# Performance work log

Hardware: AMD Instinct MI355X
Metric: run time of the kernel (lower is better)

Reference implementation:

```python
import jax, jax.numpy as jnp
import numpy as np

B, N, FIN = 512, 256, 32   # batch, num_agents, (tgt_feat+rbt_feat)*2
H1, G, FOUT, K, ACT = 16, 8, 16, 3, 5  # compress dims, shared feat G, GF out, taps, actions


def setup_inputs() -> dict:
    key = jax.random.key(0)
    ks = jax.random.split(key, 10)
    x = jax.random.normal(ks[0], (B, N, FIN), dtype=jnp.float32)
    # GSO, scaled ~1/sqrt(N) so repeated shifts stay numerically tame
    S = jax.random.normal(ks[1], (B, N, N), dtype=jnp.float32) * (1.0 / np.sqrt(N))
    def lin(k, fout, fin):
        return jax.random.normal(k, (fout, fin), dtype=jnp.float32) * (1.0 / np.sqrt(fin))
    W1, b1 = lin(ks[2], H1, FIN), jnp.zeros((H1,), jnp.float32)
    W2, b2 = lin(ks[3], G, H1), jnp.zeros((G,), jnp.float32)
    # graph-filter taps: [FOUT, K, G] (E=1 folded away)
    Hgf = jax.random.normal(ks[4], (FOUT, K, G), dtype=jnp.float32) * (1.0 / np.sqrt(K * G))
    bgf = jnp.zeros((FOUT,), jnp.float32)
    Wa, ba = lin(ks[5], ACT, FOUT), jnp.zeros((ACT,), jnp.float32)
    return {"x": x, "S": S, "W1": W1, "b1": b1, "W2": W2, "b2": b2,
            "Hgf": Hgf, "bgf": bgf, "Wa": Wa, "ba": ba}


def reference(x, S, W1, b1, W2, b2, Hgf, bgf, Wa, ba):
    # compress MLP, batched over all agents at once (replaces the per-agent loop)
    h = jax.nn.relu(jnp.einsum('bnf,hf->bnh', x, W1) + b1)
    h = jax.nn.relu(jnp.einsum('bnh,gh->bng', h, W2) + b2)   # [B, N, G]
    z = jnp.transpose(h, (0, 2, 1))                          # [B, G, N]
    # K-tap graph shift: z_k = z_{k-1} @ S
    taps = [z]
    for _ in range(K - 1):
        taps.append(jnp.einsum('bgn,bnm->bgm', taps[-1], S))
    zK = jnp.stack(taps, axis=1)                             # [B, K, G, N]
    y = jnp.einsum('fkg,bkgn->bfn', Hgf, zK) + bgf[None, :, None]
    y = jax.nn.relu(y)                                       # [B, FOUT, N]
    # action MLP per agent (single linear, batched over agents)
    actions = jnp.einsum('bfn,af->bna', y, Wa) + ba          # [B, N, ACT]
    return actions
```

## Files before the change

kernel.cpp:

```cpp
#include <hip/hip_runtime.h>

constexpr int Bsz  = 512;
constexpr int Nn   = 256;
constexpr int FINc = 32;
constexpr int H1c  = 16;
constexpr int Gc   = 8;
constexpr int FOUTc= 16;
constexpr int Kc   = 3;
constexpr int ACTc = 5;

__global__ __launch_bounds__(256, 2)
void cpn_kernel(const float* __restrict__ x,  const float* __restrict__ S,
                const float* __restrict__ W1, const float* __restrict__ b1,
                const float* __restrict__ W2, const float* __restrict__ b2,
                const float* __restrict__ Hgf,const float* __restrict__ bgf,
                const float* __restrict__ Wa, const float* __restrict__ ba,
                float* __restrict__ out)
{
    const int b    = blockIdx.x;
    const int tid  = threadIdx.x;
    const int wid  = tid >> 6;
    const int lane = tid & 63;
    const int n    = tid;

    __shared__ __align__(16) float zA[Nn][Gc];
    __shared__ __align__(16) float zB[Nn][Gc];
    __shared__ __align__(16) float zpart[4][Gc][Nn];

    float xr[FINc];
    {
        const float4* xp = reinterpret_cast<const float4*>(x + ((size_t)b * Nn + n) * FINc);
        #pragma unroll
        for (int i = 0; i < FINc / 4; ++i) {
            float4 v = xp[i];
            xr[4*i+0] = v.x; xr[4*i+1] = v.y; xr[4*i+2] = v.z; xr[4*i+3] = v.w;
        }
    }
    float h1v[H1c];
    #pragma unroll
    for (int h = 0; h < H1c; ++h) {
        float a = b1[h];
        #pragma unroll
        for (int f = 0; f < FINc; ++f) a = fmaf(W1[h*FINc + f], xr[f], a);
        h1v[h] = fmaxf(a, 0.0f);
    }
    float z0r[Gc];
    #pragma unroll
    for (int g = 0; g < Gc; ++g) {
        float a = b2[g];
        #pragma unroll
        for (int h = 0; h < H1c; ++h) a = fmaf(W2[g*H1c + h], h1v[h], a);
        z0r[g] = fmaxf(a, 0.0f);
        zA[n][g] = z0r[g];
    }
    __syncthreads();

    float z1r[Gc], z2r[Gc];

    auto spass = [&](const float (*zsrc)[Gc], float* zred) {
        float acc[Gc][4];
        #pragma unroll
        for (int g = 0; g < Gc; ++g) {
            #pragma unroll
            for (int j = 0; j < 4; ++j) acc[g][j] = 0.0f;
        }
        const float* srow = S + ((size_t)b * Nn + wid * 64) * Nn + 4 * lane;
        #pragma unroll 8
        for (int i = 0; i < 64; ++i) {
            const float4 sv = *reinterpret_cast<const float4*>(srow);
            srow += Nn;
            const int nn = wid * 64 + i;
            const float4 za = *reinterpret_cast<const float4*>(&zsrc[nn][0]);
            const float4 zb = *reinterpret_cast<const float4*>(&zsrc[nn][4]);
            const float zg[Gc] = {za.x, za.y, za.z, za.w, zb.x, zb.y, zb.z, zb.w};
            #pragma unroll
            for (int g = 0; g < Gc; ++g) {
                acc[g][0] = fmaf(zg[g], sv.x, acc[g][0]);
                acc[g][1] = fmaf(zg[g], sv.y, acc[g][1]);
                acc[g][2] = fmaf(zg[g], sv.z, acc[g][2]);
                acc[g][3] = fmaf(zg[g], sv.w, acc[g][3]);
            }
        }
        #pragma unroll
        for (int g = 0; g < Gc; ++g) {
            *reinterpret_cast<float4*>(&zpart[wid][g][4*lane]) =
                make_float4(acc[g][0], acc[g][1], acc[g][2], acc[g][3]);
        }
        __syncthreads();
        #pragma unroll
        for (int g = 0; g < Gc; ++g) {
            zred[g] = (zpart[0][g][n] + zpart[1][g][n]) + (zpart[2][g][n] + zpart[3][g][n]);
        }
    };

    spass(zA, z1r);
    #pragma unroll
    for (int g = 0; g < Gc; ++g) zB[n][g] = z1r[g];
    __syncthreads();
    spass(zB, z2r);

    float y[FOUTc];
    #pragma unroll
    for (int f = 0; f < FOUTc; ++f) y[f] = bgf[f];
    #pragma unroll
    for (int g = 0; g < Gc; ++g) {
        const float zv = z0r[g];
        #pragma unroll
        for (int f = 0; f < FOUTc; ++f) y[f] = fmaf(Hgf[f*(Kc*Gc) + 0*Gc + g], zv, y[f]);
    }
    #pragma unroll
    for (int g = 0; g < Gc; ++g) {
        const float zv = z1r[g];
        #pragma unroll
        for (int f = 0; f < FOUTc; ++f) y[f] = fmaf(Hgf[f*(Kc*Gc) + 1*Gc + g], zv, y[f]);
    }
    #pragma unroll
    for (int g = 0; g < Gc; ++g) {
        const float zv = z2r[g];
        #pragma unroll
        for (int f = 0; f < FOUTc; ++f) y[f] = fmaf(Hgf[f*(Kc*Gc) + 2*Gc + g], zv, y[f]);
    }
    #pragma unroll
    for (int f = 0; f < FOUTc; ++f) y[f] = fmaxf(y[f], 0.0f);

    float* op = out + ((size_t)b * Nn + n) * ACTc;
    #pragma unroll
    for (int a = 0; a < ACTc; ++a) {
        float acc = ba[a];
        #pragma unroll
        for (int f = 0; f < FOUTc; ++f) acc = fmaf(Wa[a*FOUTc + f], y[f], acc);
        op[a] = acc;
    }
}

extern "C" void kernel_launch(void* const* d_in, const int* in_sizes, int n_in,
                              void* d_out, int out_size, void* d_ws, size_t ws_size,
                              hipStream_t stream) {
    const float* x   = (const float*)d_in[0];
    const float* S   = (const float*)d_in[1];
    const float* W1  = (const float*)d_in[2];
    const float* b1  = (const float*)d_in[3];
    const float* W2  = (const float*)d_in[4];
    const float* b2  = (const float*)d_in[5];
    const float* Hgf = (const float*)d_in[6];
    const float* bgf = (const float*)d_in[7];
    const float* Wa  = (const float*)d_in[8];
    const float* ba  = (const float*)d_in[9];

    cpn_kernel<<<dim3(Bsz), dim3(Nn), 0, stream>>>(
        x, S, W1, b1, W2, b2, Hgf, bgf, Wa, ba, (float*)d_out);
}
```

Baseline: 57.39 us.

## Process two batches per 512-thread block with staggered S-pass pipeline

Each block now handles two batch items with 512 threads. The S-shift passes of the two batches are staggered so that one half of the block runs a pass for one batch while the other half runs the next pass for the other, and the reduction and output stages are interleaved between them. This aims to hide the serial dependency between the two graph-shift passes and the idle barriers, at the cost of half as many blocks, twice the shared memory per block, and some phases where only half the threads do work.

```diff
diff --git a/kernel.cpp b/kernel.cpp
--- a/kernel.cpp
+++ b/kernel.cpp
@@ -9,7 +9,7 @@
 constexpr int Kc   = 3;
 constexpr int ACTc = 5;
 
-__global__ __launch_bounds__(256, 2)
+__global__ __launch_bounds__(512, 2)
 void cpn_kernel(const float* __restrict__ x,  const float* __restrict__ S,
                 const float* __restrict__ W1, const float* __restrict__ b1,
                 const float* __restrict__ W2, const float* __restrict__ b2,
@@ -17,59 +17,62 @@
                 const float* __restrict__ Wa, const float* __restrict__ ba,
                 float* __restrict__ out)
 {
-    const int b    = blockIdx.x;
+    const int blk  = blockIdx.x;
+    const int bb0  = blk;
+    const int bb1  = blk + 256;
     const int tid  = threadIdx.x;
     const int wid  = tid >> 6;
     const int lane = tid & 63;
-    const int n    = tid;
 
-    __shared__ __align__(16) float zA[Nn][Gc];
-    __shared__ __align__(16) float zB[Nn][Gc];
-    __shared__ __align__(16) float zpart[4][Gc][Nn];
+    __shared__ __align__(16) float zA0[Nn][Gc], zA1[Nn][Gc];
+    __shared__ __align__(16) float zB0[Nn][Gc], zB1[Nn][Gc];
+    __shared__ __align__(16) float zpA[4][Gc][Nn], zpB[4][Gc][Nn];
 
-    float xr[FINc];
     {
-        const float4* xp = reinterpret_cast<const float4*>(x + ((size_t)b * Nn + n) * FINc);
+        const int sel = tid >> 8;
+        const int n   = tid & 255;
+        const int bb  = sel ? bb1 : bb0;
+        float (*zdst)[Gc] = sel ? zA1 : zA0;
+
+        float xr[FINc];
+        const float4* xp = reinterpret_cast<const float4*>(x + ((size_t)bb * Nn + n) * FINc);
         #pragma unroll
         for (int i = 0; i < FINc / 4; ++i) {
             float4 v = xp[i];
             xr[4*i+0] = v.x; xr[4*i+1] = v.y; xr[4*i+2] = v.z; xr[4*i+3] = v.w;
         }
-    }
-    float h1v[H1c];
-    #pragma unroll
-    for (int h = 0; h < H1c; ++h) {
-        float a = b1[h];
+        float h1v[H1c];
         #pragma unroll
-        for (int f = 0; f < FINc; ++f) a = fmaf(W1[h*FINc + f], xr[f], a);
-        h1v[h] = fmaxf(a, 0.0f);
-    }
-    float z0r[Gc];
-    #pragma unroll
-    for (int g = 0; g < Gc; ++g) {
-        float a = b2[g];
+        for (int h = 0; h < H1c; ++h) {
+            float a = b1[h];
+            #pragma unroll
+            for (int f = 0; f < FINc; ++f) a = fmaf(W1[h*FINc + f], xr[f], a);
+            h1v[h] = fmaxf(a, 0.0f);
+        }
         #pragma unroll
-        for (int h = 0; h < H1c; ++h) a = fmaf(W2[g*H1c + h], h1v[h], a);
-        z0r[g] = fmaxf(a, 0.0f);
-        zA[n][g] = z0r[g];
+        for (int g = 0; g < Gc; ++g) {
+            float a = b2[g];
+            #pragma unroll
+            for (int h = 0; h < H1c; ++h) a = fmaf(W2[g*H1c + h], h1v[h], a);
+            zdst[n][g] = fmaxf(a, 0.0f);
+        }
     }
     __syncthreads();
 
-    float z1r[Gc], z2r[Gc];
-
-    auto spass = [&](const float (*zsrc)[Gc], float* zred) {
+    auto spass4 = [&](const float (*zsrc)[Gc], float (*zp)[Gc][Nn],
+                      const float* sbatch, int wg4) {
         float acc[Gc][4];
         #pragma unroll
-        for (int g = 0; g < Gc; ++g) {
+        for (int g = 0; g < Gc; ++g)
             #pragma unroll
             for (int j = 0; j < 4; ++j) acc[g][j] = 0.0f;
-        }
-        const float* srow = S + ((size_t)b * Nn + wid * 64) * Nn + 4 * lane;
+
+        const float* srow = sbatch + (size_t)(wg4 * 64) * Nn + 4 * lane;
         #pragma unroll 8
         for (int i = 0; i < 64; ++i) {
             const float4 sv = *reinterpret_cast<const float4*>(srow);
             srow += Nn;
-            const int nn = wid * 64 + i;
+            const int nn = wg4 * 64 + i;
             const float4 za = *reinterpret_cast<const float4*>(&zsrc[nn][0]);
             const float4 zb = *reinterpret_cast<const float4*>(&zsrc[nn][4]);
             const float zg[Gc] = {za.x, za.y, za.z, za.w, zb.x, zb.y, zb.z, zb.w};
@@ -82,54 +85,88 @@
             }
         }
         #pragma unroll
-        for (int g = 0; g < Gc; ++g) {
-            *reinterpret_cast<float4*>(&zpart[wid][g][4*lane]) =
+        for (int g = 0; g < Gc; ++g)
+            *reinterpret_cast<float4*>(&zp[wg4][g][4 * lane]) =
                 make_float4(acc[g][0], acc[g][1], acc[g][2], acc[g][3]);
-        }
-        __syncthreads();
+    };
+
+    auto merge_pub = [&](const float (*zp)[Gc][Nn], float (*zdst)[Gc], int n) {
+        #pragma unroll
+        for (int g = 0; g < Gc; ++g)
+            zdst[n][g] = (zp[0][g][n] + zp[1][g][n]) + (zp[2][g][n] + zp[3][g][n]);
+    };
+    auto merge_reg = [&](const float (*zp)[Gc][Nn], float* zr, int n) {
+        #pragma unroll
+        for (int g = 0; g < Gc; ++g)
+            zr[g] = (zp[0][g][n] + zp[1][g][n]) + (zp[2][g][n] + zp[3][g][n]);
+    };
+    auto phaseC = [&](int bb, int n, const float (*z0s)[Gc], const float (*z1s)[Gc],
+                      const float* z2r) {
+        const float4 a0 = *reinterpret_cast<const float4*>(&z0s[n][0]);
+        const float4 a1 = *reinterpret_cast<const float4*>(&z0s[n][4]);
+        const float4 c0 = *reinterpret_cast<const float4*>(&z1s[n][0]);
+        const float4 c1 = *reinterpret_cast<const float4*>(&z1s[n][4]);
+        const float z0g[Gc] = {a0.x, a0.y, a0.z, a0.w, a1.x, a1.y, a1.z, a1.w};
+        const float z1g[Gc] = {c0.x, c0.y, c0.z, c0.w, c1.x, c1.y, c1.z, c1.w};
+
+        float y[FOUTc];
+        #pragma unroll
+        for (int f = 0; f < FOUTc; ++f) y[f] = bgf[f];
         #pragma unroll
         for (int g = 0; g < Gc; ++g) {
-            zred[g] = (zpart[0][g][n] + zpart[1][g][n]) + (zpart[2][g][n] + zpart[3][g][n]);
+            #pragma unroll
+            for (int f = 0; f < FOUTc; ++f) y[f] = fmaf(Hgf[f*(Kc*Gc) + 0*Gc + g], z0g[g], y[f]);
+        }
+        #pragma unroll
+        for (int g = 0; g < Gc; ++g) {
+            #pragma unroll
+            for (int f = 0; f < FOUTc; ++f) y[f] = fmaf(Hgf[f*(Kc*Gc) + 1*Gc + g], z1g[g], y[f]);
+        }
+        #pragma unroll
+        for (int g = 0; g < Gc; ++g) {
+            #pragma unroll
+            for (int f = 0; f < FOUTc; ++f) y[f] = fmaf(Hgf[f*(Kc*Gc) + 2*Gc + g], z2r[g], y[f]);
+        }
+        #pragma unroll
+        for (int f = 0; f < FOUTc; ++f) y[f] = fmaxf(y[f], 0.0f);
+
+        float* op = out + ((size_t)bb * Nn + n) * ACTc;
+        #pragma unroll
+        for (int a = 0; a < ACTc; ++a) {
+            float acc = ba[a];
+            #pragma unroll
+            for (int f = 0; f < FOUTc; ++f) acc = fmaf(Wa[a*FOUTc + f], y[f], acc);
+            op[a] = acc;
         }
     };
 
-    spass(zA, z1r);
-    #pragma unroll
-    for (int g = 0; g < Gc; ++g) zB[n][g] = z1r[g];
+    const float* S0p = S + (size_t)bb0 * Nn * Nn;
+    const float* S1p = S + (size_t)bb1 * Nn * Nn;
+
+    if (wid < 4) spass4(zA0, zpA, S0p, wid);
     __syncthreads();
-    spass(zB, z2r);
+    if (tid < Nn) merge_pub(zpA, zB0, tid);
+    __syncthreads();
 
-    float y[FOUTc];
-    #pragma unroll
-    for (int f = 0; f < FOUTc; ++f) y[f] = bgf[f];
-    #pragma unroll
-    for (int g = 0; g < Gc; ++g) {
-        const float zv = z0r[g];
-        #pragma unroll
-        for (int f = 0; f < FOUTc; ++f) y[f] = fmaf(Hgf[f*(Kc*Gc) + 0*Gc + g], zv, y[f]);
+    if (wid < 4) spass4(zA1, zpB, S1p, wid);
+    else         spass4(zB0, zpA, S0p, wid - 4);
+    __syncthreads();
+    if (tid < Nn) {
+        merge_pub(zpB, zB1, tid);
+    } else {
+        const int n = tid - Nn;
+        float z2r[Gc];
+        merge_reg(zpA, z2r, n);
+        phaseC(bb0, n, zA0, zB0, z2r);
     }
-    #pragma unroll
-    for (int g = 0; g < Gc; ++g) {
-        const float zv = z1r[g];
-        #pragma unroll
-        for (int f = 0; f < FOUTc; ++f) y[f] = fmaf(Hgf[f*(Kc*Gc) + 1*Gc + g], zv, y[f]);
-    }
-    #pragma unroll
-    for (int g = 0; g < Gc; ++g) {
-        const float zv = z2r[g];
-        #pragma unroll
-        for (int f = 0; f < FOUTc; ++f) y[f] = fmaf(Hgf[f*(Kc*Gc) + 2*Gc + g], zv, y[f]);
-    }
-    #pragma unroll
-    for (int f = 0; f < FOUTc; ++f) y[f] = fmaxf(y[f], 0.0f);
+    __syncthreads();
 
-    float* op = out + ((size_t)b * Nn + n) * ACTc;
-    #pragma unroll
-    for (int a = 0; a < ACTc; ++a) {
-        float acc = ba[a];
-        #pragma unroll
-        for (int f = 0; f < FOUTc; ++f) acc = fmaf(Wa[a*FOUTc + f], y[f], acc);
-        op[a] = acc;
+    if (wid < 4) spass4(zB1, zpB, S1p, wid);
+    __syncthreads();
+    if (tid < Nn) {
+        float z2r[Gc];
+        merge_reg(zpB, z2r, tid);
+        phaseC(bb1, tid, zA1, zB1, z2r);
     }
 }
 
@@ -147,6 +184,6 @@
     const float* Wa  = (const float*)d_in[8];
     const float* ba  = (const float*)d_in[9];
 
-    cpn_kernel<<<dim3(Bsz), dim3(Nn), 0, stream>>>(
+    cpn_kernel<<<dim3(Bsz / 2), dim3(512), 0, stream>>>(
         x, S, W1, b1, W2, b2, Hgf, bgf, Wa, ba, (float*)d_out);
 }
```

Measured after the change: 57.25 us. No clear change (-0.2%).
